# Kernel optimization log

Hardware: AMD Instinct MI355X
Metric: run time of the kernel (lower is better)

Reference implementation:

```python
import jax, jax.numpy as jnp
import numpy as np

B, T_ENC, T_DEC = 16, 128, 100
IN_DIM, HIDDEN, OUT_DIM, MEM_DIM, BUF_LEN = 256, 256, 400, 80, 17
BUF_DIM = IN_DIM + MEM_DIM          # 336
BUF_SIZE = BUF_LEN * BUF_DIM        # 5712


def setup_inputs() -> dict:
    key = jax.random.key(0)
    ks = jax.random.split(key, 12)
    def rn(k, shape, scale=0.05):
        return jax.random.normal(k, shape, dtype=jnp.float32) * scale
    return {
        "inputs": jax.random.normal(ks[0], (B, T_ENC, IN_DIM), jnp.float32),
        "targets": jax.random.normal(ks[1], (B, T_DEC, OUT_DIM), jnp.float32),
        "mp_w1": rn(ks[2], (OUT_DIM, OUT_DIM // 10)), "mp_b1": jnp.zeros((OUT_DIM // 10,), jnp.float32),
        "mp_w2": rn(ks[3], (OUT_DIM // 10, MEM_DIM)), "mp_b2": jnp.zeros((MEM_DIM,), jnp.float32),
        "bp_w1": rn(ks[4], (BUF_SIZE, BUF_SIZE // 10)), "bp_b1": jnp.zeros((BUF_SIZE // 10,), jnp.float32),
        "bp_w2": rn(ks[5], (BUF_SIZE // 10, BUF_DIM)), "bp_b2": jnp.zeros((BUF_DIM,), jnp.float32),
        "att_wq": rn(ks[6], (BUF_SIZE, HIDDEN)), "att_bq": jnp.zeros((HIDDEN,), jnp.float32),
        "att_wa": rn(ks[7], (IN_DIM, HIDDEN)), "att_ba": jnp.zeros((HIDDEN,), jnp.float32),
        "att_v": rn(ks[8], (HIDDEN,)),
        "scale_w": rn(ks[9], (HIDDEN, BUF_DIM)), "scale_b": jnp.zeros((HIDDEN,), jnp.float32),
        "out_w": rn(ks[10], (HIDDEN * BUF_LEN, OUT_DIM)), "out_b": jnp.zeros((OUT_DIM,), jnp.float32),
    }


def _decode(inputs, targets, mp_w1, mp_b1, mp_w2, mp_b2, bp_w1, bp_b1, bp_w2, bp_b2,
            att_wq, att_bq, att_wa, att_ba, att_v, scale_w, scale_b, out_w, out_b):
    b = inputs.shape[0]
    # Bahdanau attention: processed annotations (constant across decode steps)
    pa = inputs @ att_wa + att_ba                               # (B, T_enc, H)
    # Teacher forcing: memory at step t is targets[t-1], zeros at t=0.
    mems = jnp.concatenate([jnp.zeros_like(targets[:, :1]), targets[:, :-1]], axis=1)
    mems = jnp.swapaxes(mems, 0, 1)                             # (T_dec, B, out_dim)
    buf0 = jnp.zeros((b, BUF_LEN, BUF_DIM), inputs.dtype)

    def step(buf, mem):
        # memory projection MLP (out_dim -> out_dim//10 -> memory_dim)
        mem_p = jax.nn.relu(mem @ mp_w1 + mp_b1) @ mp_w2 + mp_b2            # (B, mem)
        # attention with flattened buffer as query
        pq = buf.reshape(b, -1) @ att_wq + att_bq                           # (B, H)
        scores = jnp.tanh(pq[:, None, :] + pa) @ att_v                      # (B, T_enc)
        attn = jax.nn.softmax(scores, axis=-1)
        ctx = jnp.einsum('bt,bti->bi', attn, inputs)                        # (B, in_dim)
        # buffer update: project [new_frame; old_buffer[:-1]] and shift in
        top = jnp.concatenate([ctx, mem_p], axis=1)[:, None, :]             # (B,1,buf_dim)
        z = jnp.concatenate([top, buf[:, :-1]], axis=1)                     # (B,L,buf_dim)
        u = jax.nn.relu(z.reshape(b, -1) @ bp_w1 + bp_b1) @ bp_w2 + bp_b2   # (B,buf_dim)
        buf = jnp.concatenate([u[:, None, :], buf[:, :-1]], axis=1)
        # Conv1dBank: Conv1dBlock.forward returns the (scaled) input, so the
        # effective op is the 1x1 'scale' conv of block0 (buf_dim -> hidden);
        # blocks 1 and 2 have in_features == out_features and pass x through.
        h = jnp.einsum('bld,hd->blh', buf, scale_w) + scale_b               # (B,L,H)
        out = h.reshape(b, -1) @ out_w + out_b                              # (B,out_dim)
        return buf, (out, attn)

    _, (outs, attns) = jax.lax.scan(step, buf0, mems)
    return jnp.swapaxes(outs, 0, 1), jnp.swapaxes(attns, 0, 1)


def reference(inputs, targets, mp_w1, mp_b1, mp_w2, mp_b2, bp_w1, bp_b1, bp_w2, bp_b2,
              att_wq, att_bq, att_wa, att_ba, att_v, scale_w, scale_b, out_w, out_b):
    return _decode(inputs, targets, mp_w1, mp_b1, mp_w2, mp_b2, bp_w1, bp_b1, bp_w2, bp_b2,
                   att_wq, att_bq, att_wa, att_ba, att_v, scale_w, scale_b, out_w, out_b)
```

## Files before the change

### kernel.cpp

```cpp
#include <hip/hip_runtime.h>

#define B     16
#define TENC  128
#define TDEC  100
#define IND   256
#define HID   256
#define OD    400
#define MD    80
#define LBUF  17
#define BD    336
#define BS    5712
#define BH    571
#define MH    40
#define NSLOT 117

#define NA    117
#define NT    18
#define NU2   28
#define NC    16
#define NBLK  (NA+NT+NU2+NC)

#define OFF_U    0
#define OFF_UT   628992
#define OFF_PA   1257984
#define OFF_MEM  1782272
#define OFF_M    1910272
#define OFF_CO   4195072
#define OFF_W2T  4195472
#define OFF_P    4387664
#define OFF_TOPT 4440912
#define OFF_H    4451664
#define OFF_FLG  4470096

#define RLX __ATOMIC_RELAXED
#define AGT __HIP_MEMORY_SCOPE_AGENT
#define SCLD(p)    __hip_atomic_load((p), RLX, AGT)
#define SCST(p,v)  __hip_atomic_store((p), (v), RLX, AGT)

__global__ __launch_bounds__(256) void k_init(float* __restrict__ ws) {
    int i = blockIdx.x*256 + threadIdx.x;
    if (i < 91392) ws[OFF_U + i] = 0.f;
    else if (i < 182784) ws[OFF_UT + (i - 91392)] = 0.f;
    else if (i < 183184) ws[OFF_CO + (i - 182784)] = 0.f;
    else if (i < 236432) ws[OFF_P + (i - 183184)] = 0.f;
    else if (i < 236944) ((int*)(ws + OFF_FLG))[i - 236432] = 0;
}

__global__ __launch_bounds__(256) void k_pa(const float* __restrict__ inputs,
        const float* __restrict__ wa, const float* __restrict__ ba,
        float* __restrict__ ws) {
    int bj = blockIdx.x;
    int tid = threadIdx.x;
    __shared__ float xin[IND];
    xin[tid] = inputs[bj*IND + tid];
    __syncthreads();
    float acc = ba[tid];
    #pragma unroll 4
    for (int i = 0; i < IND; i++) acc += xin[i]*wa[i*HID + tid];
    ws[OFF_PA + bj*HID + tid] = acc;
}

__global__ __launch_bounds__(128) void k_mem(const float* __restrict__ targets,
        const float* __restrict__ w1, const float* __restrict__ b1,
        const float* __restrict__ w2, const float* __restrict__ b2,
        float* __restrict__ ws) {
    int tb = blockIdx.x; int t = tb / B; int b = tb % B;
    int tid = threadIdx.x;
    __shared__ float xin[OD];
    __shared__ float hid[MH];
    for (int k = tid; k < OD; k += 128)
        xin[k] = (t == 0) ? 0.f : targets[(b*TDEC + (t-1))*OD + k];
    __syncthreads();
    if (tid < MH) {
        float a = b1[tid];
        for (int k = 0; k < OD; k++) a += xin[k]*w1[k*MH + tid];
        hid[tid] = fmaxf(a, 0.f);
    }
    __syncthreads();
    if (tid < MD) {
        float a = b2[tid];
        #pragma unroll
        for (int k = 0; k < MH; k++) a += hid[k]*w2[k*MD + tid];
        ws[OFF_MEM + (t*B + b)*MD + tid] = a;
    }
}

__global__ __launch_bounds__(256) void k_M(const float* __restrict__ scale_w,
        const float* __restrict__ out_w, float* __restrict__ ws) {
    int l  = blockIdx.x / 14;
    int d0 = (blockIdx.x % 14) * 24;
    int tid = threadIdx.x;
    __shared__ float sw[HID*24];
    for (int idx = tid; idx < HID*24; idx += 256) {
        int h = idx / 24, dl = idx % 24;
        sw[idx] = scale_w[h*BD + d0 + dl];
    }
    __syncthreads();
    int o0 = tid, o1 = tid + 256;
    bool v1 = o1 < OD;
    float a0[24], a1[24];
    #pragma unroll
    for (int i = 0; i < 24; i++) { a0[i] = 0.f; a1[i] = 0.f; }
    const float* owl = out_w + l*HID*OD;
    for (int h = 0; h < HID; h++) {
        float w0 = owl[h*OD + o0];
        float w1v = v1 ? owl[h*OD + o1] : 0.f;
        #pragma unroll
        for (int dl = 0; dl < 24; dl++) {
            float s = sw[h*24 + dl];
            a0[dl] += s*w0; a1[dl] += s*w1v;
        }
    }
    float* Mp = ws + OFF_M + l*BD*OD;
    for (int dl = 0; dl < 24; dl++) {
        Mp[(d0+dl)*OD + o0] = a0[dl];
        if (v1) Mp[(d0+dl)*OD + o1] = a1[dl];
    }
}

__global__ __launch_bounds__(256) void k_cout(const float* __restrict__ scale_b,
        const float* __restrict__ out_w, const float* __restrict__ out_b,
        float* __restrict__ ws) {
    int l = blockIdx.x; int tid = threadIdx.x;
    for (int p = 0; p < 2; p++) {
        int o = tid + p*256;
        if (o < OD) {
            float acc = (l == 0) ? out_b[o] : 0.f;
            for (int h = 0; h < HID; h++) acc += scale_b[h]*out_w[(l*HID + h)*OD + o];
            atomicAdd(&ws[OFF_CO + o], acc);
        }
    }
}

__global__ __launch_bounds__(256) void k_tr(const float* __restrict__ bp_w2,
        float* __restrict__ ws) {
    int i = blockIdx.x*256 + threadIdx.x;
    if (i < BD*572) {
        int dd = i / 572, c = i - 572*dd;
        ws[OFF_W2T + i] = (c < BH) ? bp_w2[c*BD + dd] : 0.f;
    }
}

__global__ __launch_bounds__(512) void k_scan(
        const float* __restrict__ inputs, const float* __restrict__ wq,
        const float* __restrict__ w1g, const float* __restrict__ att_bq,
        const float* __restrict__ bp_b1, const float* __restrict__ bp_b2,
        const float* __restrict__ att_v,
        float* __restrict__ ws, float* __restrict__ attns) {
    __shared__ __align__(16) float smem[16128];
    int bid = blockIdx.x, tid = threadIdx.x;
    int* AF = (int*)(ws + OFF_FLG);
    int* CF = AF + 128;
    int* TF = AF + 160;
    int* UF = AF + 192;

    if (bid < NA) {
        int a_lo, n_ages, ct;
        if (bid < 13) { a_lo = 1; n_ages = 1; ct = bid; }
        else { int q = bid - 13; int p = q/13; ct = q - 13*p; a_lo = 2 + 2*p; n_ages = 2; }
        float* ulds = smem;
        float* red  = smem + 5376;
        int cp = tid & 31, kq = tid >> 5;
        int c0 = ct*64 + cp, c1 = c0 + 32;
        float wA[2][21], wB[2][21];
        for (int ia = 0; ia < 2; ia++) {
            int a = a_lo + ia;
            #pragma unroll
            for (int g = 0; g < 21; g++) {
                int d = kq*21 + g;
                float va = 0.f, vb = 0.f;
                if (ia < n_ages) {
                    va = (c0 < 256) ? wq[((a-1)*336+d)*256 + c0]
                       : ((a <= 16 && c0 < 827) ? w1g[(a*336+d)*BH + (c0-256)] : 0.f);
                    vb = (c1 < 256) ? wq[((a-1)*336+d)*256 + c1]
                       : ((a <= 16 && c1 < 827) ? w1g[(a*336+d)*BH + (c1-256)] : 0.f);
                }
                wA[ia][g] = va; wB[ia][g] = vb;
            }
        }
        int aw = (a_lo < 4) ? a_lo : 4;
        for (int t = 0; t < TDEC; t++) {
            int s = t - aw;
            if (s >= 0) {
                for (;;) {
                    int p = 1;
                    if (tid < NU2) p = (SCLD(&UF[tid]) >= s+1);
                    if (__syncthreads_count(p) == 512) break;
                    __builtin_amdgcn_s_sleep(1);
                }
            }
            float a0[16], a1[16];
            #pragma unroll
            for (int i = 0; i < 16; i++) { a0[i] = 0.f; a1[i] = 0.f; }
            for (int ia = 0; ia < n_ages; ia++) {
                int a = a_lo + ia;
                if (ia) __syncthreads();
                {
                    const float* src = ws + OFF_UT + (t + 17 - a)*5376;
                    float r[11];
                    #pragma unroll
                    for (int j = 0; j < 10; j++) r[j] = SCLD(&src[tid + j*512]);
                    if (tid < 256) r[10] = SCLD(&src[tid + 5120]);
                    #pragma unroll
                    for (int j = 0; j < 10; j++) ulds[tid + j*512] = r[j];
                    if (tid < 256) ulds[tid + 5120] = r[10];
                }
                __syncthreads();
                #pragma unroll
                for (int g = 0; g < 21; g++) {
                    int base = (kq*21 + g)*16;
                    float4 u0 = *(const float4*)&ulds[base];
                    float4 u1 = *(const float4*)&ulds[base+4];
                    float4 u2 = *(const float4*)&ulds[base+8];
                    float4 u3 = *(const float4*)&ulds[base+12];
                    float wa = wA[ia][g], wb = wB[ia][g];
                    a0[0]=fmaf(wa,u0.x,a0[0]);  a1[0]=fmaf(wb,u0.x,a1[0]);
                    a0[1]=fmaf(wa,u0.y,a0[1]);  a1[1]=fmaf(wb,u0.y,a1[1]);
                    a0[2]=fmaf(wa,u0.z,a0[2]);  a1[2]=fmaf(wb,u0.z,a1[2]);
                    a0[3]=fmaf(wa,u0.w,a0[3]);  a1[3]=fmaf(wb,u0.w,a1[3]);
                    a0[4]=fmaf(wa,u1.x,a0[4]);  a1[4]=fmaf(wb,u1.x,a1[4]);
                    a0[5]=fmaf(wa,u1.y,a0[5]);  a1[5]=fmaf(wb,u1.y,a1[5]);
                    a0[6]=fmaf(wa,u1.z,a0[6]);  a1[6]=fmaf(wb,u1.z,a1[6]);
                    a0[7]=fmaf(wa,u1.w,a0[7]);  a1[7]=fmaf(wb,u1.w,a1[7]);
                    a0[8]=fmaf(wa,u2.x,a0[8]);  a1[8]=fmaf(wb,u2.x,a1[8]);
                    a0[9]=fmaf(wa,u2.y,a0[9]);  a1[9]=fmaf(wb,u2.y,a1[9]);
                    a0[10]=fmaf(wa,u2.z,a0[10]); a1[10]=fmaf(wb,u2.z,a1[10]);
                    a0[11]=fmaf(wa,u2.w,a0[11]); a1[11]=fmaf(wb,u2.w,a1[11]);
                    a0[12]=fmaf(wa,u3.x,a0[12]); a1[12]=fmaf(wb,u3.x,a1[12]);
                    a0[13]=fmaf(wa,u3.y,a0[13]); a1[13]=fmaf(wb,u3.y,a1[13]);
                    a0[14]=fmaf(wa,u3.z,a0[14]); a1[14]=fmaf(wb,u3.z,a1[14]);
                    a0[15]=fmaf(wa,u3.w,a0[15]); a1[15]=fmaf(wb,u3.w,a1[15]);
                }
            }
            if (kq < 8) {
                #pragma unroll
                for (int bb = 0; bb < 16; bb++) {
                    red[kq*1024 + bb*64 + cp]      = a0[bb];
                    red[kq*1024 + bb*64 + cp + 32] = a1[bb];
                }
            }
            __syncthreads();
            if (kq >= 8) {
                #pragma unroll
                for (int bb = 0; bb < 16; bb++) {
                    red[(kq-8)*1024 + bb*64 + cp]      += a0[bb];
                    red[(kq-8)*1024 + bb*64 + cp + 32] += a1[bb];
                }
            }
            __syncthreads();
            int par = t & 3;
            for (int oi = tid; oi < 1024; oi += 512) {
                float s_ = 0.f;
                #pragma unroll
                for (int q = 0; q < 8; q++) s_ += red[q*1024 + oi];
                int bb = oi >> 6, cl = oi & 63;
                __hip_atomic_fetch_add(
                    &ws[OFF_P + ((par*B + bb)*832) + ct*64 + cl], s_, RLX, AGT);
            }
            __syncthreads();
            if (tid == 0) SCST(&AF[bid], t + 1);
        }
    } else if (bid < NA + NT) {
        int f = bid - NA;
        float* w1L  = smem;
        float* tlds = smem + 10752;
        for (int idx = tid; idx < 10752; idx += 512) {
            int d = idx >> 5, c = idx & 31;
            int col = f*32 + c;
            w1L[idx] = (col < BH) ? w1g[d*BH + col] : 0.f;
        }
        __syncthreads();
        int cl = tid >> 4, b = tid & 15;
        int col = f*32 + cl;
        for (int t = 0; t < TDEC; t++) {
            for (;;) {
                int p = 1;
                if (tid < NC) p = (SCLD(&CF[tid]) >= t+1);
                if (__syncthreads_count(p) == 512) break;
                __builtin_amdgcn_s_sleep(1);
            }
            int par2 = t & 1;
            float prime = SCLD(&ws[OFF_H + par2*9216 + f*512 + tid]);
            {
                const float* src = ws + OFF_TOPT + par2*5376;
                float r[11];
                #pragma unroll
                for (int j = 0; j < 10; j++) r[j] = SCLD(&src[tid + j*512]);
                if (tid < 256) r[10] = SCLD(&src[tid + 5120]);
                #pragma unroll
                for (int j = 0; j < 10; j++) tlds[tid + j*512] = r[j];
                if (tid < 256) tlds[tid + 5120] = r[10];
            }
            __syncthreads();
            float acc = 0.f;
            const float* wrow = w1L + cl;
            const float* trow = tlds + b;
            #pragma unroll 8
            for (int d = 0; d < 336; d++)
                acc = fmaf(trow[d*16], wrow[d*32], acc);
            if (col < BH)
                SCST(&ws[OFF_H + par2*9216 + f*512 + tid], fmaxf(prime + acc, 0.f));
            __syncthreads();
            if (tid == 0) SCST(&TF[f], t + 1);
        }
    } else if (bid < NA + NT + NU2) {
        int ub = bid - (NA + NT);
        int dd0 = ub*12;
        float* w2L  = smem;
        float* hlds = smem + 6864;
        for (int idx = tid; idx < 6864; idx += 512)
            w2L[idx] = ws[OFF_W2T + dd0*572 + idx];
        __syncthreads();
        int ddl = tid >> 4, b = tid & 15;
        bool act = tid < 192;
        for (int t = 0; t < TDEC; t++) {
            for (;;) {
                int p = 1;
                if (tid < NT) p = (SCLD(&TF[tid]) >= t+1);
                if (__syncthreads_count(p) == 512) break;
                __builtin_amdgcn_s_sleep(1);
            }
            int par2 = t & 1;
            {
                const float* src = ws + OFF_H + par2*9216;
                float r[18];
                #pragma unroll
                for (int j = 0; j < 18; j++) {
                    int idx = tid + j*512;
                    r[j] = (idx < 9136) ? SCLD(&src[idx]) : 0.f;
                }
                #pragma unroll
                for (int j = 0; j < 18; j++) {
                    int idx = tid + j*512;
                    if (idx < 9136) hlds[idx] = r[j];
                }
            }
            __syncthreads();
            if (act) {
                float v = bp_b2[dd0 + ddl];
                const float* wrow = w2L + ddl*572;
                const float* hrow = hlds + b;
                #pragma unroll 8
                for (int c = 0; c < BH; c++)
                    v = fmaf(hrow[c*16], wrow[c], v);
                SCST(&ws[OFF_U + ((t+17)*B + b)*BD + dd0 + ddl], v);
                SCST(&ws[OFF_UT + (t+17)*5376 + (dd0+ddl)*16 + b], v);
            }
            __syncthreads();
            if (tid == 0) SCST(&UF[ub], t + 1);
        }
    } else {
        int b = bid - (NA + NT + NU2);
        float* pqa    = smem;
        float* sc     = smem + 832;
        float* attn_s = smem + 960;
        float* ctx2   = smem + 1088;
        float* topv   = smem + 1600;
        float* avs    = smem + 1936;
        if (tid < 256) avs[tid] = att_v[tid];
        __syncthreads();
        for (int t = 0; t < TDEC; t++) {
            for (;;) {
                int p = 1;
                if (tid < NA) p = (SCLD(&AF[tid]) >= t+1);
                if (__syncthreads_count(p) == 512) break;
                __builtin_amdgcn_s_sleep(1);
            }
            int par3 = t & 3, par2 = t & 1;
            {
                float* Pb = ws + OFF_P + (par3*B + b)*832;
                int c0 = tid;
                float p0 = SCLD(&Pb[c0]);
                SCST(&Pb[c0], 0.f);
                pqa[c0] = p0 + (c0 < 256 ? att_bq[c0] : bp_b1[c0-256]);
                if (tid < 315) {
                    int c1 = tid + 512;
                    float p1 = SCLD(&Pb[c1]);
                    SCST(&Pb[c1], 0.f);
                    pqa[c1] = p1 + bp_b1[c1-256];
                }
            }
            __syncthreads();
            {
                int j = tid >> 2, hq = tid & 3;
                const float* par_ = ws + OFF_PA + (b*TENC + j)*HID + hq*64;
                const float* pqh = &pqa[hq*64];
                const float* avh = &avs[hq*64];
                float a = 0.f;
                #pragma unroll 8
                for (int h = 0; h < 64; h++) {
                    float x = pqh[h] + par_[h];
                    float e = __expf(2.f*x);
                    a += avh[h]*(1.f - 2.f/(e + 1.f));
                }
                a += __shfl_xor(a, 1);
                a += __shfl_xor(a, 2);
                if (hq == 0) sc[j] = a;
            }
            __syncthreads();
            if (tid < 64) {
                float s0 = sc[2*tid], s1 = sc[2*tid+1];
                float m = fmaxf(s0, s1);
                #pragma unroll
                for (int off = 1; off < 64; off <<= 1) m = fmaxf(m, __shfl_xor(m, off));
                float e0 = __expf(s0 - m), e1 = __expf(s1 - m);
                float ssum = e0 + e1;
                #pragma unroll
                for (int off = 1; off < 64; off <<= 1) ssum += __shfl_xor(ssum, off);
                float r = 1.f/ssum;
                attn_s[2*tid] = e0*r; attn_s[2*tid+1] = e1*r;
                attns[(b*TDEC + t)*TENC + 2*tid]   = e0*r;
                attns[(b*TDEC + t)*TENC + 2*tid+1] = e1*r;
            }
            __syncthreads();
            {
                int i = tid & 255, jh = tid >> 8;
                const float* inp = inputs + (b*TENC + jh*64)*IND + i;
                float csum = 0.f;
                #pragma unroll 8
                for (int j = 0; j < 64; j++)
                    csum += attn_s[jh*64 + j]*inp[j*IND];
                ctx2[jh*256 + i] = csum;
            }
            __syncthreads();
            if (tid < 256) topv[tid] = ctx2[tid] + ctx2[256 + tid];
            else if (tid < BD) topv[tid] = ws[OFF_MEM + (t*B + b)*MD + (tid-256)];
            __syncthreads();
            if (tid < BD)
                SCST(&ws[OFF_TOPT + par2*5376 + tid*16 + b], topv[tid]);
            SCST(&ws[OFF_H + par2*9216 + tid*16 + b], pqa[256 + tid]);
            if (tid < 59)
                SCST(&ws[OFF_H + par2*9216 + (tid+512)*16 + b], pqa[256 + tid + 512]);
            __syncthreads();
            if (tid == 0) SCST(&CF[b], t + 1);
        }
    }
}

__global__ __launch_bounds__(256) void k_q2(float* __restrict__ outs,
        const float* __restrict__ ws) {
    __shared__ __align__(16) float uL[41*340];
    int bid = blockIdx.x;
    int b = bid >> 5, r = bid & 31, th = r >> 3, oc = r & 7;
    int t0 = th*25, obase = oc*50;
    int tid = threadIdx.x;
    int s0 = t0 + 1;
    for (int idx = tid; idx < 41*336; idx += 256) {
        int rr = idx / 336, d = idx - 336*rr;
        uL[rr*340 + d] = ws[OFF_U + ((s0 + rr)*B + b)*BD + d];
    }
    __syncthreads();
    int o = tid % 50, tq = tid / 50;
    if (tq < 5) {
        float acc[5] = {0.f, 0.f, 0.f, 0.f, 0.f};
        for (int l = 0; l < LBUF; l++) {
            const float* Mp = ws + OFF_M + (l*BD)*OD + obase + o;
            const float* ub = &uL[(tq*5 + 16 - l)*340];
            for (int d4 = 0; d4 < 84; d4++) {
                int d = d4*4;
                float m0 = Mp[(d+0)*OD], m1 = Mp[(d+1)*OD];
                float m2 = Mp[(d+2)*OD], m3 = Mp[(d+3)*OD];
                #pragma unroll
                for (int i = 0; i < 5; i++) {
                    float4 u4 = *(const float4*)&ub[i*340 + d];
                    acc[i] = fmaf(u4.x, m0, acc[i]);
                    acc[i] = fmaf(u4.y, m1, acc[i]);
                    acc[i] = fmaf(u4.z, m2, acc[i]);
                    acc[i] = fmaf(u4.w, m3, acc[i]);
                }
            }
        }
        float co = ws[OFF_CO + obase + o];
        #pragma unroll
        for (int i = 0; i < 5; i++) {
            int t = t0 + tq*5 + i;
            outs[(b*TDEC + t)*OD + obase + o] = acc[i] + co;
        }
    }
}

extern "C" void kernel_launch(void* const* d_in, const int* in_sizes, int n_in,
                              void* d_out, int out_size, void* d_ws, size_t ws_size,
                              hipStream_t stream) {
    const float* inputs  = (const float*)d_in[0];
    const float* targets = (const float*)d_in[1];
    const float* mp_w1   = (const float*)d_in[2];
    const float* mp_b1   = (const float*)d_in[3];
    const float* mp_w2   = (const float*)d_in[4];
    const float* mp_b2   = (const float*)d_in[5];
    const float* bp_w1   = (const float*)d_in[6];
    const float* bp_b1   = (const float*)d_in[7];
    const float* bp_w2   = (const float*)d_in[8];
    const float* bp_b2   = (const float*)d_in[9];
    const float* att_wq  = (const float*)d_in[10];
    const float* att_bq  = (const float*)d_in[11];
    const float* att_wa  = (const float*)d_in[12];
    const float* att_ba  = (const float*)d_in[13];
    const float* att_v   = (const float*)d_in[14];
    const float* scale_w = (const float*)d_in[15];
    const float* scale_b = (const float*)d_in[16];
    const float* out_w   = (const float*)d_in[17];
    const float* out_b   = (const float*)d_in[18];
    float* ws = (float*)d_ws;
    float* outs = (float*)d_out;
    float* attns = outs + B*TDEC*OD;

    k_init<<<926, 256, 0, stream>>>(ws);
    k_pa  <<<B*TENC, 256, 0, stream>>>(inputs, att_wa, att_ba, ws);
    k_mem <<<TDEC*B, 128, 0, stream>>>(targets, mp_w1, mp_b1, mp_w2, mp_b2, ws);
    k_M   <<<17*14, 256, 0, stream>>>(scale_w, out_w, ws);
    k_cout<<<17, 256, 0, stream>>>(scale_b, out_w, out_b, ws);
    k_tr  <<<(BD*572 + 255)/256, 256, 0, stream>>>(bp_w2, ws);
    k_scan<<<NBLK, 512, 0, stream>>>(inputs, att_wq, bp_w1, att_bq, bp_b1,
                                     bp_b2, att_v, ws, attns);
    k_q2  <<<512, 256, 0, stream>>>(outs, ws);
}
```

Baseline: 4.177 ms.

## Drop transposed U copy; transpose in LDS and switch to row-major global buffers

```diff
diff --git a/kernel.cpp b/kernel.cpp
--- a/kernel.cpp
+++ b/kernel.cpp
@@ -21,16 +21,15 @@
 #define NBLK  (NA+NT+NU2+NC)
 
 #define OFF_U    0
-#define OFF_UT   628992
-#define OFF_PA   1257984
-#define OFF_MEM  1782272
-#define OFF_M    1910272
-#define OFF_CO   4195072
-#define OFF_W2T  4195472
-#define OFF_P    4387664
-#define OFF_TOPT 4440912
-#define OFF_H    4451664
-#define OFF_FLG  4470096
+#define OFF_PA   628992
+#define OFF_MEM  1153280
+#define OFF_M    1281280
+#define OFF_CO   3566080
+#define OFF_W2T  3566480
+#define OFF_P    3758672
+#define OFF_TOP  3811920
+#define OFF_H    3822672
+#define OFF_FLG  3840976
 
 #define RLX __ATOMIC_RELAXED
 #define AGT __HIP_MEMORY_SCOPE_AGENT
@@ -40,10 +39,9 @@
 __global__ __launch_bounds__(256) void k_init(float* __restrict__ ws) {
     int i = blockIdx.x*256 + threadIdx.x;
     if (i < 91392) ws[OFF_U + i] = 0.f;
-    else if (i < 182784) ws[OFF_UT + (i - 91392)] = 0.f;
-    else if (i < 183184) ws[OFF_CO + (i - 182784)] = 0.f;
-    else if (i < 236432) ws[OFF_P + (i - 183184)] = 0.f;
-    else if (i < 236944) ((int*)(ws + OFF_FLG))[i - 236432] = 0;
+    else if (i < 91792) ws[OFF_CO + (i - 91392)] = 0.f;
+    else if (i < 145040) ws[OFF_P + (i - 91792)] = 0.f;
+    else if (i < 145552) ((int*)(ws + OFF_FLG))[i - 145040] = 0;
 }
 
 __global__ __launch_bounds__(256) void k_pa(const float* __restrict__ inputs,
@@ -147,7 +145,7 @@
         const float* __restrict__ bp_b1, const float* __restrict__ bp_b2,
         const float* __restrict__ att_v,
         float* __restrict__ ws, float* __restrict__ attns) {
-    __shared__ __align__(16) float smem[16128];
+    __shared__ __align__(16) float smem[16192];
     int bid = blockIdx.x, tid = threadIdx.x;
     int* AF = (int*)(ws + OFF_FLG);
     int* CF = AF + 128;
@@ -159,7 +157,7 @@
         if (bid < 13) { a_lo = 1; n_ages = 1; ct = bid; }
         else { int q = bid - 13; int p = q/13; ct = q - 13*p; a_lo = 2 + 2*p; n_ages = 2; }
         float* ulds = smem;
-        float* red  = smem + 5376;
+        float* red  = smem + 6720;
         int cp = tid & 31, kq = tid >> 5;
         int c0 = ct*64 + cp, c1 = c0 + 32;
         float wA[2][21], wB[2][21];
@@ -196,19 +194,27 @@
                 int a = a_lo + ia;
                 if (ia) __syncthreads();
                 {
-                    const float* src = ws + OFF_UT + (t + 17 - a)*5376;
+                    const float* src = ws + OFF_U + (t + 17 - a)*5376;
                     float r[11];
                     #pragma unroll
                     for (int j = 0; j < 10; j++) r[j] = SCLD(&src[tid + j*512]);
                     if (tid < 256) r[10] = SCLD(&src[tid + 5120]);
                     #pragma unroll
-                    for (int j = 0; j < 10; j++) ulds[tid + j*512] = r[j];
-                    if (tid < 256) ulds[tid + 5120] = r[10];
+                    for (int j = 0; j < 10; j++) {
+                        int idx = tid + j*512;
+                        int b = idx/336, d = idx - 336*b;
+                        ulds[d*20 + b] = r[j];
+                    }
+                    if (tid < 256) {
+                        int idx = tid + 5120;
+                        int b = idx/336, d = idx - 336*b;
+                        ulds[d*20 + b] = r[10];
+                    }
                 }
                 __syncthreads();
                 #pragma unroll
                 for (int g = 0; g < 21; g++) {
-                    int base = (kq*21 + g)*16;
+                    int base = (kq*21 + g)*20;
                     float4 u0 = *(const float4*)&ulds[base];
                     float4 u1 = *(const float4*)&ulds[base+4];
                     float4 u2 = *(const float4*)&ulds[base+8];
@@ -262,16 +268,17 @@
         }
     } else if (bid < NA + NT) {
         int f = bid - NA;
-        float* w1L  = smem;
+        float* w1T  = smem;
         float* tlds = smem + 10752;
         for (int idx = tid; idx < 10752; idx += 512) {
             int d = idx >> 5, c = idx & 31;
             int col = f*32 + c;
-            w1L[idx] = (col < BH) ? w1g[d*BH + col] : 0.f;
+            w1T[c*336 + d] = (col < BH) ? w1g[d*BH + col] : 0.f;
         }
         __syncthreads();
         int cl = tid >> 4, b = tid & 15;
         int col = f*32 + cl;
+        bool val = col < BH;
         for (int t = 0; t < TDEC; t++) {
             for (;;) {
                 int p = 1;
@@ -280,26 +287,37 @@
                 __builtin_amdgcn_s_sleep(1);
             }
             int par2 = t & 1;
-            float prime = SCLD(&ws[OFF_H + par2*9216 + f*512 + tid]);
+            float prime = val ? SCLD(&ws[OFF_H + par2*9152 + b*572 + col]) : 0.f;
             {
-                const float* src = ws + OFF_TOPT + par2*5376;
+                const float* src = ws + OFF_TOP + par2*5376;
                 float r[11];
                 #pragma unroll
                 for (int j = 0; j < 10; j++) r[j] = SCLD(&src[tid + j*512]);
                 if (tid < 256) r[10] = SCLD(&src[tid + 5120]);
                 #pragma unroll
-                for (int j = 0; j < 10; j++) tlds[tid + j*512] = r[j];
-                if (tid < 256) tlds[tid + 5120] = r[10];
+                for (int j = 0; j < 10; j++) {
+                    int idx = tid + j*512;
+                    int bb = idx/336, d = idx - 336*bb;
+                    tlds[bb*340 + d] = r[j];
+                }
+                if (tid < 256) {
+                    int idx = tid + 5120;
+                    int bb = idx/336, d = idx - 336*bb;
+                    tlds[bb*340 + d] = r[10];
+                }
             }
             __syncthreads();
             float acc = 0.f;
-            const float* wrow = w1L + cl;
-            const float* trow = tlds + b;
+            const float4* tp = (const float4*)&tlds[b*340];
+            const float4* wp = (const float4*)&w1T[cl*336];
             #pragma unroll 8
-            for (int d = 0; d < 336; d++)
-                acc = fmaf(trow[d*16], wrow[d*32], acc);
-            if (col < BH)
-                SCST(&ws[OFF_H + par2*9216 + f*512 + tid], fmaxf(prime + acc, 0.f));
+            for (int q = 0; q < 84; q++) {
+                float4 tv = tp[q], wv = wp[q];
+                acc = fmaf(tv.x, wv.x, acc); acc = fmaf(tv.y, wv.y, acc);
+                acc = fmaf(tv.z, wv.z, acc); acc = fmaf(tv.w, wv.w, acc);
+            }
+            if (val)
+                SCST(&ws[OFF_H + par2*9152 + b*572 + col], fmaxf(prime + acc, 0.f));
             __syncthreads();
             if (tid == 0) SCST(&TF[f], t + 1);
         }
@@ -322,29 +340,31 @@
             }
             int par2 = t & 1;
             {
-                const float* src = ws + OFF_H + par2*9216;
+                const float* src = ws + OFF_H + par2*9152;
                 float r[18];
                 #pragma unroll
                 for (int j = 0; j < 18; j++) {
                     int idx = tid + j*512;
-                    r[j] = (idx < 9136) ? SCLD(&src[idx]) : 0.f;
+                    r[j] = (idx < 9152) ? SCLD(&src[idx]) : 0.f;
                 }
                 #pragma unroll
                 for (int j = 0; j < 18; j++) {
                     int idx = tid + j*512;
-                    if (idx < 9136) hlds[idx] = r[j];
+                    if (idx < 9152) hlds[idx] = r[j];
                 }
             }
             __syncthreads();
             if (act) {
                 float v = bp_b2[dd0 + ddl];
-                const float* wrow = w2L + ddl*572;
-                const float* hrow = hlds + b;
+                const float4* hp = (const float4*)&hlds[b*572];
+                const float4* wp = (const float4*)&w2L[ddl*572];
                 #pragma unroll 8
-                for (int c = 0; c < BH; c++)
-                    v = fmaf(hrow[c*16], wrow[c], v);
+                for (int q = 0; q < 143; q++) {
+                    float4 hh = hp[q], wv = wp[q];
+                    v = fmaf(hh.x, wv.x, v); v = fmaf(hh.y, wv.y, v);
+                    v = fmaf(hh.z, wv.z, v); v = fmaf(hh.w, wv.w, v);
+                }
                 SCST(&ws[OFF_U + ((t+17)*B + b)*BD + dd0 + ddl], v);
-                SCST(&ws[OFF_UT + (t+17)*5376 + (dd0+ddl)*16 + b], v);
             }
             __syncthreads();
             if (tid == 0) SCST(&UF[ub], t + 1);
@@ -427,10 +447,12 @@
             else if (tid < BD) topv[tid] = ws[OFF_MEM + (t*B + b)*MD + (tid-256)];
             __syncthreads();
             if (tid < BD)
-                SCST(&ws[OFF_TOPT + par2*5376 + tid*16 + b], topv[tid]);
-            SCST(&ws[OFF_H + par2*9216 + tid*16 + b], pqa[256 + tid]);
+                SCST(&ws[OFF_TOP + par2*5376 + b*336 + tid], topv[tid]);
+            SCST(&ws[OFF_H + par2*9152 + b*572 + tid], pqa[256 + tid]);
             if (tid < 59)
-                SCST(&ws[OFF_H + par2*9216 + (tid+512)*16 + b], pqa[256 + tid + 512]);
+                SCST(&ws[OFF_H + par2*9152 + b*572 + 512 + tid], pqa[256 + 512 + tid]);
+            if (tid == 0)
+                SCST(&ws[OFF_H + par2*9152 + b*572 + 571], 0.f);
             __syncthreads();
             if (tid == 0) SCST(&CF[b], t + 1);
         }
@@ -505,7 +527,7 @@
     float* outs = (float*)d_out;
     float* attns = outs + B*TDEC*OD;
 
-    k_init<<<926, 256, 0, stream>>>(ws);
+    k_init<<<569, 256, 0, stream>>>(ws);
     k_pa  <<<B*TENC, 256, 0, stream>>>(inputs, att_wa, att_ba, ws);
     k_mem <<<TDEC*B, 128, 0, stream>>>(targets, mp_w1, mp_b1, mp_w2, mp_b2, ws);
     k_M   <<<17*14, 256, 0, stream>>>(scale_w, out_w, ws);
```

New measurement: 3.522 ms. -15.7%, faster.
